# Performance work log

Measured on AMD Instinct MI355X. Metric: run time of the kernel, lower is better.

## Reference

```python
import math
import jax, jax.numpy as jnp
import numpy as np

B, S, DIM = 2, 4096, 512
HEADS, DIM_HEAD, CHUNK = 8, 64, 64
DIM_INNER = HEADS * DIM_HEAD
EPS = 1e-6


def rmsnorm(x, scale):
    var = jnp.mean(x * x, axis=-1, keepdims=True)
    return x * jax.lax.rsqrt(var + EPS) * scale


def mem_attn(p, x):
    # x: [c, dh] single chunk; tiny causal attention memory model
    q = x @ p['wq']
    k = x @ p['wk']
    v = x @ p['wv1']
    d = q.shape[-1]
    dots = (q @ k.T) * (d ** -0.5)
    c = x.shape[-2]
    mask = jnp.tril(jnp.ones((c, c), dtype=bool))
    dots = jnp.where(mask, dots, -1e9)
    attn = jax.nn.softmax(dots, axis=-1)
    hidden = attn @ v
    return jax.nn.silu(hidden) @ p['wv2']


def mem_loss(p, inp, tgt):
    pred = mem_attn(p, inp)
    return jnp.sum(jnp.mean((pred - tgt) ** 2, axis=-1))


def assoc_scan(gates, vals):
    # first-order linear recurrence y_t = g_t * y_{t-1} + v_t along axis=1
    def op(a, b):
        a1, b1 = a
        a2, b2 = b
        return a1 * a2, a2 * b1 + b2
    return jax.lax.associative_scan(op, (gates, vals), axis=1)


def setup_inputs():
    key = jax.random.key(0)
    ks = jax.random.split(key, 16)
    n = lambda k, shp, s: jax.random.normal(k, shp, dtype=jnp.float32) * s
    return {
        'seq': n(ks[0], (B, S, DIM), 1.0),
        'w_store_norm': jnp.ones((DIM,), jnp.float32),
        'w_retrieve_norm': jnp.ones((DIM,), jnp.float32),
        'w_post_norm': jnp.ones((DIM,), jnp.float32),
        'w_q': n(ks[1], (DIM, DIM_INNER), DIM ** -0.5),
        'w_kv': n(ks[2], (DIM, 2 * DIM_INNER), DIM ** -0.5),
        'w_step': n(ks[3], (DIM, HEADS), DIM ** -0.5),
        'w_mom': n(ks[4], (DIM, HEADS), DIM ** -0.5),
        'w_decay': n(ks[5], (DIM, HEADS), DIM ** -0.5),
        'w_combine': n(ks[6], (DIM_INNER, DIM), DIM_INNER ** -0.5),
        'wq': n(ks[7], (DIM_HEAD, DIM_HEAD), 0.01),
        'wk': n(ks[8], (DIM_HEAD, DIM_HEAD), 0.01),
        'wv1': n(ks[9], (DIM_HEAD, DIM_HEAD), 0.01),
        'wv2': n(ks[10], (DIM_HEAD, DIM_HEAD), 0.01),
    }


def reference(seq, w_store_norm, w_retrieve_norm, w_post_norm, w_q, w_kv,
              w_step, w_mom, w_decay, w_combine, wq, wk, wv1, wv2):
    b, s_len, d = seq.shape
    c, h, dh = CHUNK, HEADS, DIM_HEAD
    past = {'wq': wq, 'wk': wk, 'wv1': wv1, 'wv2': wv2}

    # ---------- store_memories ----------
    s = rmsnorm(seq, w_store_norm)
    n_full = (s_len // c) * c
    s = s[:, :n_full]
    nc = n_full // c

    # adaptive lr: [b,n,h] -> (b h) n -> chunk-mean [bh, nc]
    lr = jnp.exp(jax.nn.sigmoid(s @ w_step) * -15.0)
    lr = jnp.transpose(lr, (0, 2, 1)).reshape(b * h, nc, c).mean(-1)

    s_mean = s.reshape(b, nc, c, d).mean(2)  # [b, nc, d]
    mom_gate = jax.nn.sigmoid(s_mean @ w_mom)
    mom_gate = jnp.transpose(mom_gate, (0, 2, 1)).reshape(b * h, nc, 1)
    decay = jax.nn.sigmoid(s_mean @ w_decay)
    decay = jnp.transpose(decay, (0, 2, 1)).reshape(b * h, nc, 1)

    keys, values = jnp.split(s @ w_kv, 2, axis=-1)

    def chunkify(t):  # [b, n, h*dh] -> [(b h nc), c, dh]
        t = t.reshape(b, n_full, h, dh)
        t = jnp.transpose(t, (0, 2, 1, 3))
        return t.reshape(b * h * nc, c, dh)

    keys, values = chunkify(keys), chunkify(values)

    # per-chunk meta-gradients wrt shared memory-model params
    grads = jax.vmap(jax.grad(mem_loss), in_axes=(None, 0, 0))(past, keys, values)

    updates = {}
    for name in past:
        g = grads[name].reshape(b * h, nc, dh * dh)
        surprise = g * (-lr)[..., None]
        _, momentum = assoc_scan(mom_gate, surprise)
        _, upd = assoc_scan(1.0 - decay, momentum)
        updates[name] = upd.reshape(b * h, nc, dh, dh)

    wwu = {k2: past[k2][None, None] + updates[k2] for k2 in past}  # [bh, nc, dh, dh]

    # ---------- retrieve_memories ----------
    r = rmsnorm(seq, w_retrieve_norm)
    rc = r[:, c:]
    curtailed = s_len - c
    next_len = ((curtailed + 1 + c - 1) // c) * c
    pad = next_len - curtailed
    rc = jnp.pad(rc, ((0, 0), (0, pad), (0, 0)))

    q = rc @ w_q  # [b, next_len, h*dh]
    q = q.reshape(b, next_len, h, dh)
    q = jnp.transpose(q, (0, 2, 1, 3)).reshape(b * h * (next_len // c), c, dh)

    pc = {k2: v2.reshape(b * h * nc, dh, dh) for k2, v2 in wwu.items()}
    vals = jax.vmap(mem_attn)(pc, q)  # [(bh nc), c, dh]
    vals = vals.reshape(b, h, next_len, dh)
    vals = jnp.transpose(vals, (0, 2, 1, 3)).reshape(b, next_len, h * dh)
    vals = rmsnorm(vals @ w_combine, w_post_norm)
    vals = jnp.pad(vals, ((0, 0), (c, 0), (0, 0)))
    return vals[:, :-pad]
```

## Files before the change

kernel.cpp:

```cpp
#include <hip/hip_runtime.h>
#include <math.h>

constexpr int BATCH = 2, SEQ = 4096, DIM = 512, HEADS = 8, DH = 64, CH = 64;
constexpr int NC = SEQ / CH;
constexpr int BH = BATCH * HEADS;
constexpr int NCHUNK = BH * NC;
constexpr int ROWS = BATCH * SEQ;
constexpr int DI = HEADS * DH;
constexpr int TS = 64 * 72;

typedef __attribute__((ext_vector_type(8))) short short8;
typedef __attribute__((ext_vector_type(4))) short short4v;
typedef __attribute__((ext_vector_type(4))) float f32x4;

__device__ inline float sigmoidf_(float x){ return 1.f/(1.f+__expf(-x)); }
__device__ inline float dsilu_f(float x){ float s = sigmoidf_(x); return s*(1.f + x*(1.f-s)); }

__device__ inline unsigned short f2b(float f){
  union { float f; unsigned int u; } c; c.f = f;
  unsigned int u = c.u;
  unsigned int r = (u + 0x7FFFu + ((u >> 16) & 1u)) >> 16;
  return (unsigned short)r;
}
__device__ inline float b2f(unsigned short h){
// ... 12 lines not shown

template<bool SILUA>
__device__ inline void mm64(const unsigned short* A, const unsigned short* B,
                            f32x4 (&acc)[2], const MM& m)
{
  acc[0] = (f32x4){0.f,0.f,0.f,0.f};
  acc[1] = (f32x4){0.f,0.f,0.f,0.f};
  #pragma unroll
  for (int ks = 0; ks < 2; ks++){
    short8 a = *(const short8*)&A[(m.rowbase + m.lr)*72 + ks*32 + m.lg*8];
    if constexpr (SILUA){
      #pragma unroll
      for (int j = 0; j < 8; j++){
        float v = b2f((unsigned short)a[j]);
        v = v * sigmoidf_(v);
        a[j] = (short)f2b(v);
      }
    }
    #pragma unroll
    for (int ct = 0; ct < 2; ct++){
      short8 b = *(const short8*)&B[(m.colbase + ct*16 + m.lr)*72 + ks*32 + m.lg*8];
      acc[ct] = __builtin_amdgcn_mfma_f32_16x16x32_bf16(a, b, acc[ct], 0, 0, 0);
    }
  }
}

__device__ inline void storeN64(unsigned short* R, const f32x4 (&acc)[2], const MM& m, float scale){
  #pragma unroll
  for (int ct = 0; ct < 2; ct++){
    int c  = m.colbase + ct*16 + m.lr;
    int mb = m.rowbase + m.lg*4;
    #pragma unroll
    for (int r = 0; r < 4; r++) R[(mb+r)*72 + c] = f2b(acc[ct][r] * scale);
  }
}
__device__ inline void storeT64(unsigned short* T, const f32x4 (&acc)[2], const MM& m, float scale){
  #pragma unroll
  for (int ct = 0; ct < 2; ct++){
    int c  = m.colbase + ct*16 + m.lr;
    int mb = m.rowbase + m.lg*4;
    short4v p;
    #pragma unroll
    for (int r = 0; r < 4; r++) p[r] = (short)f2b(acc[ct][r] * scale);
    *(short4v*)&T[c*72 + mb] = p;
  }
}
__device__ inline void storeSC(float* S, const f32x4 (&acc)[2], const MM& m, float scale){
  #pragma unroll
  for (int ct = 0; ct < 2; ct++){
    int c  = m.colbase + ct*16 + m.lr;
    int mb = m.rowbase + m.lg*4;
    #pragma unroll
    for (int r = 0; r < 4; r++) S[(mb+r)*66 + c] = acc[ct][r] * scale;
  }
}
__device__ inline void storeGTb64(unsigned short* __restrict__ G, const f32x4 (&acc)[2],
                                  const MM& m, float scale){
  #pragma unroll
  for (int ct = 0; ct < 2; ct++){
    int c  = m.colbase + ct*16 + m.lr;
    int mb = m.rowbase + m.lg*4;
    short4v p;
    #pragma unroll
    for (int r = 0; r < 4; r++) p[r] = (short)f2b(acc[ct][r] * scale);
    *(short4v*)&G[c*64 + mb] = p;
  }
}

__device__ inline void loadTileBrow(unsigned short* R, const unsigned short* __restrict__ src,
                                    int stride, int tid){
  int i = tid >> 3, j8 = (tid & 7) * 8;
  *(short8*)&R[i*72 + j8] = *(const short8*)&src[(size_t)i*stride + j8];
}
__device__ inline void loadTileBrowT(unsigned short* R, unsigned short* T,
                                     const unsigned short* __restrict__ src,
                                     int stride, int tid){
  int i = tid >> 3, j8 = (tid & 7) * 8;
  short8 v = *(const short8*)&src[(size_t)i*stride + j8];
  *(short8*)&R[i*72 + j8] = v;
  #pragma unroll
  for (int jj = 0; jj < 8; jj++) T[(j8+jj)*72 + i] = (unsigned short)v[jj];
}

__global__ __launch_bounds__(256) void k_wprep_all(
    const float* __restrict__ w_kv, const float* __restrict__ w_q,
    const float* __restrict__ wcomb,
    const float* __restrict__ wq, const float* __restrict__ wk,
    const float* __restrict__ wv1, const float* __restrict__ wv2,
    unsigned short* __restrict__ wkvT_hi, unsigned short* __restrict__ wkvT_lo,
    unsigned short* __restrict__ wqT_hi, unsigned short* __restrict__ wcombT_hi,
    unsigned short* __restrict__ wpre)
{
  __shared__ float t[64][65];
  int blk = blockIdx.x;
  int tid = threadIdx.x;
  if (blk < 256){
    const float* src; unsigned short *dhi, *dlo;
    int R, C, bx, by;
    if (blk < 128){ src = w_kv;  dhi = wkvT_hi;  dlo = wkvT_lo; R = DIM; C = 2*DI; bx = blk & 15; by = blk >> 4; }
    else if (blk < 192){ int q = blk - 128; src = w_q;   dhi = wqT_hi;    dlo = nullptr; R = DIM; C = DI;  bx = q & 7; by = q >> 3; }
    else               { int q = blk - 192; src = wcomb; dhi = wcombT_hi; dlo = nullptr; R = DI;  C = DIM; bx = q & 7; by = q >> 3; }
    int c0 = bx * 64, r0 = by * 64;
    #pragma unroll
    for (int it = 0; it < 16; it++){
      int idx = it*256 + tid;
      int i = idx >> 6, j = idx & 63;
      t[i][j] = src[(size_t)(r0+i)*C + c0 + j];
    }
    __syncthreads();
    #pragma unroll
    for (int it = 0; it < 16; it++){
      int idx = it*256 + tid;
      int i = idx >> 6, j = idx & 63;
      float v = t[j][i];
      unsigned short hi = f2b(v);
      dhi[(size_t)(c0+i)*R + r0 + j] = hi;
      if (dlo) dlo[(size_t)(c0+i)*R + r0 + j] = f2b(v - b2f(hi));
    }
  } else {
    int b = blk - 256;
    const float* src = (b==0) ? wq : (b==1) ? wk : (b==2) ? wv1 : wv2;
    #pragma unroll
    for (int it = 0; it < 16; it++){
      int idx = it*256 + tid;
      int i = idx >> 6, j = idx & 63;
      t[i][j] = src[i*64 + j];
    }
    __syncthreads();
    #pragma unroll
    for (int it = 0; it < 16; it++){
      int idx = it*256 + tid;
      int i = idx >> 6, j = idx & 63;
      wpre[b*4096 + i*64 + j] = f2b(t[j][i]);
      if (b == 3) wpre[4*4096 + i*64 + j] = f2b(t[i][j]);
    }
  }
}

template<int MODE, bool LO>
__global__ __launch_bounds__(256, LO ? 2 : 4) void k_gemm3(
    const unsigned short* __restrict__ Ahg, const unsigned short* __restrict__ Alg,
    const unsigned short* __restrict__ Bhg, const unsigned short* __restrict__ Blg,
    float* __restrict__ Cf, unsigned short* __restrict__ Cb, int M, int N, int K)
{
  __shared__ __align__(16) unsigned short AhS[128*72];
  __shared__ __align__(16) unsigned short BhS[128*72];
  __shared__ __align__(16) unsigned short AlS[LO ? 128*72 : 8];
  __shared__ __align__(16) unsigned short BlS[LO ? 128*72 : 8];
  int tid = threadIdx.x;
  int nwg = gridDim.x * gridDim.y;
  int bid = blockIdx.y * gridDim.x + blockIdx.x;
  int swz = (bid & 7) * (nwg >> 3) + (bid >> 3);
  int m0 = (swz / gridDim.x) * 128;
  int n0 = (swz % gridDim.x) * 128;
  int wid = tid >> 6, lane = tid & 63;
  int lr = lane & 15, lg = lane >> 4;
  int wr = (wid >> 1) * 64, wc = (wid & 1) * 64;
  f32x4 acc[4][4];
  #pragma unroll
  for (int r = 0; r < 4; r++)
    #pragma unroll
    for (int c = 0; c < 4; c++) acc[r][c] = (f32x4){0.f,0.f,0.f,0.f};

  for (int k0 = 0; k0 < K; k0 += 64){
    #pragma unroll
    for (int it = 0; it < 4; it++){
      int idx = it*256 + tid;
      int row = idx >> 3, col8 = (idx & 7) * 8;
      size_t ga = (size_t)(m0+row)*K + k0 + col8;
      size_t gb = (size_t)(n0+row)*K + k0 + col8;
      *(short8*)&AhS[row*72 + col8] = *(const short8*)&Ahg[ga];
      *(short8*)&BhS[row*72 + col8] = *(const short8*)&Bhg[gb];
      if constexpr (LO){
        *(short8*)&AlS[row*72 + col8] = *(const short8*)&Alg[ga];
        *(short8*)&BlS[row*72 + col8] = *(const short8*)&Blg[gb];
      }
    }
    __syncthreads();
    #pragma unroll
    for (int ks = 0; ks < 2; ks++){
      short8 ah[4], al[4], bh[4], bl[4];
      #pragma unroll
      for (int i = 0; i < 4; i++){
        int ao = (wr + i*16 + lr)*72 + ks*32 + lg*8;
        int bo = (wc + i*16 + lr)*72 + ks*32 + lg*8;
        ah[i] = *(const short8*)&AhS[ao];
        bh[i] = *(const short8*)&BhS[bo];
        if constexpr (LO){
          al[i] = *(const short8*)&AlS[ao];
          bl[i] = *(const short8*)&BlS[bo];
        }
      }
      #pragma unroll
      for (int r = 0; r < 4; r++)
        #pragma unroll
        for (int c = 0; c < 4; c++){
          acc[r][c] = __builtin_amdgcn_mfma_f32_16x16x32_bf16(ah[r], bh[c], acc[r][c], 0, 0, 0);
          if constexpr (LO){
            acc[r][c] = __builtin_amdgcn_mfma_f32_16x16x32_bf16(ah[r], bl[c], acc[r][c], 0, 0, 0);
            acc[r][c] = __builtin_amdgcn_mfma_f32_16x16x32_bf16(al[r], bh[c], acc[r][c], 0, 0, 0);
          }
        }
    }
    __syncthreads();
  }
  #pragma unroll
  for (int rt = 0; rt < 4; rt++)
    #pragma unroll
    for (int ct = 0; ct < 4; ct++){
      int col = n0 + wc + ct*16 + lr;
      int rowb = m0 + wr + rt*16 + lg*4;
      #pragma unroll
      for (int r = 0; r < 4; r++){
        float v = acc[rt][ct][r];
        if constexpr (MODE == 0) Cf[(size_t)(rowb+r)*N + col] = v;
        if constexpr (MODE == 1) Cb[(size_t)(rowb+r)*N + col] = f2b(v);
      }
    }
}

__global__ __launch_bounds__(256, 4) void k_gemm1_dual(
    const unsigned short* __restrict__ A0, const unsigned short* __restrict__ B0,
    unsigned short* __restrict__ C0,
    const unsigned short* __restrict__ A1, const unsigned short* __restrict__ B1,
    unsigned short* __restrict__ C1, int M, int N, int K)
{
  __shared__ __align__(16) unsigned short AhS[128*72];
  __shared__ __align__(16) unsigned short BhS[128*72];
  const unsigned short* Ahg = blockIdx.z ? A1 : A0;
  const unsigned short* Bhg = blockIdx.z ? B1 : B0;
  unsigned short* Cb        = blockIdx.z ? C1 : C0;
  int tid = threadIdx.x;
  int nwg = gridDim.x * gridDim.y;
  int bid = blockIdx.y * gridDim.x + blockIdx.x;
  int swz = (bid & 7) * (nwg >> 3) + (bid >> 3);
  int m0 = (swz / gridDim.x) * 128;
  int n0 = (swz % gridDim.x) * 128;
  int wid = tid >> 6, lane = tid & 63;
  int lr = lane & 15, lg = lane >> 4;
  int wr = (wid >> 1) * 64, wc = (wid & 1) * 64;
  f32x4 acc[4][4];
  #pragma unroll
  for (int r = 0; r < 4; r++)
    #pragma unroll
    for (int c = 0; c < 4; c++) acc[r][c] = (f32x4){0.f,0.f,0.f,0.f};

  for (int k0 = 0; k0 < K; k0 += 64){
    #pragma unroll
    for (int it = 0; it < 4; it++){
      int idx = it*256 + tid;
      int row = idx >> 3, col8 = (idx & 7) * 8;
      *(short8*)&AhS[row*72 + col8] = *(const short8*)&Ahg[(size_t)(m0+row)*K + k0 + col8];
      *(short8*)&BhS[row*72 + col8] = *(const short8*)&Bhg[(size_t)(n0+row)*K + k0 + col8];
    }
    __syncthreads();
    #pragma unroll
    for (int ks = 0; ks < 2; ks++){
      short8 ah[4], bh[4];
      #pragma unroll
      for (int i = 0; i < 4; i++){
        ah[i] = *(const short8*)&AhS[(wr + i*16 + lr)*72 + ks*32 + lg*8];
        bh[i] = *(const short8*)&BhS[(wc + i*16 + lr)*72 + ks*32 + lg*8];
      }
      #pragma unroll
      for (int r = 0; r < 4; r++)
        #pragma unroll
        for (int c = 0; c < 4; c++)
          acc[r][c] = __builtin_amdgcn_mfma_f32_16x16x32_bf16(ah[r], bh[c], acc[r][c], 0, 0, 0);
    }
    __syncthreads();
  }
  #pragma unroll
  for (int rt = 0; rt < 4; rt++)
    #pragma unroll
    for (int ct = 0; ct < 4; ct++){
      int col = n0 + wc + ct*16 + lr;
      int rowb = m0 + wr + rt*16 + lg*4;
      #pragma unroll
      for (int r = 0; r < 4; r++)
        Cb[(size_t)(rowb+r)*N + col] = f2b(acc[rt][ct][r]);
    }
}

__global__ __launch_bounds__(256) void k_store_norm(
    const float* __restrict__ seq, const float* __restrict__ wsn,
    const float* __restrict__ wrn, const float* __restrict__ wstep,
    unsigned short* __restrict__ s_hi, unsigned short* __restrict__ s_lo,
    unsigned short* __restrict__ rq_hi, float* __restrict__ lrp)
{
  int wid = threadIdx.x >> 6, lane = threadIdx.x & 63;
  int row = blockIdx.x * 4 + wid;
  int b = row >> 12, t = row & 4095;
  const float* x = seq + (size_t)row * DIM;
  float4 v0 = *(const float4*)&x[lane*4];
  float4 v1 = *(const float4*)&x[256 + lane*4];
  float xv[8] = {v0.x, v0.y, v0.z, v0.w, v1.x, v1.y, v1.z, v1.w};
  float ss = 0.f;
  #pragma unroll
  for (int j = 0; j < 8; j++) ss += xv[j]*xv[j];
  #pragma unroll
  for (int m = 1; m < 64; m <<= 1) ss += __shfl_xor(ss, m);
  float rinv = rsqrtf(ss * (1.f/DIM) + 1e-6f);

  float4 w0 = *(const float4*)&wsn[lane*4];
  float4 w1 = *(const float4*)&wsn[256 + lane*4];
  float wv[8] = {w0.x, w0.y, w0.z, w0.w, w1.x, w1.y, w1.z, w1.w};
  float sv[8];
  short4v h0, h1, l0, l1;
  #pragma unroll
  for (int j = 0; j < 8; j++){
    sv[j] = xv[j] * rinv * wv[j];
    unsigned short hi = f2b(sv[j]);
    unsigned short lo = f2b(sv[j] - b2f(hi));
    if (j < 4){ h0[j] = (short)hi; l0[j] = (short)lo; }
    else      { h1[j-4] = (short)hi; l1[j-4] = (short)lo; }
  }
  size_t sbase = (size_t)row*DIM + lane*4;
  *(short4v*)&s_hi[sbase] = h0; *(short4v*)&s_hi[sbase + 256] = h1;
  *(short4v*)&s_lo[sbase] = l0; *(short4v*)&s_lo[sbase + 256] = l1;

  if (t >= CH){
    float4 r0 = *(const float4*)&wrn[lane*4];
    float4 r1 = *(const float4*)&wrn[256 + lane*4];
    float rv[8] = {r0.x, r0.y, r0.z, r0.w, r1.x, r1.y, r1.z, r1.w};
    short4v rh0, rh1;
    #pragma unroll
    for (int j = 0; j < 8; j++){
      float q = xv[j] * rinv * rv[j];
      unsigned short hi = f2b(q);
      if (j < 4) rh0[j] = (short)hi; else rh1[j-4] = (short)hi;
    }
    size_t rbase = ((size_t)b*SEQ + (t - CH))*DIM + lane*4;
    *(short4v*)&rq_hi[rbase] = rh0; *(short4v*)&rq_hi[rbase + 256] = rh1;
  } else {
    short4v z; z[0]=0; z[1]=0; z[2]=0; z[3]=0;
    size_t rbase = ((size_t)b*SEQ + (SEQ - CH + t))*DIM + lane*4;
    *(short4v*)&rq_hi[rbase] = z; *(short4v*)&rq_hi[rbase + 256] = z;
  }

  float acc[8] = {0.f,0.f,0.f,0.f,0.f,0.f,0.f,0.f};
  #pragma unroll
  for (int j = 0; j < 8; j++){
    int e = (j < 4) ? (lane*4 + j) : (256 + lane*4 + (j-4));
    float4 wa = *(const float4*)&wstep[e*8];
    float4 wb = *(const float4*)&wstep[e*8 + 4];
    acc[0] += sv[j]*wa.x; acc[1] += sv[j]*wa.y; acc[2] += sv[j]*wa.z; acc[3] += sv[j]*wa.w;
    acc[4] += sv[j]*wb.x; acc[5] += sv[j]*wb.y; acc[6] += sv[j]*wb.z; acc[7] += sv[j]*wb.w;
  }
  #pragma unroll
  for (int m = 1; m < 64; m <<= 1){
    #pragma unroll
    for (int h = 0; h < 8; h++) acc[h] += __shfl_xor(acc[h], m);
  }
  float a = acc[0];
  #pragma unroll
  for (int h = 1; h < 8; h++) a = (lane == h) ? acc[h] : a;
  if (lane < 8)
    lrp[(size_t)row*HEADS + lane] = __expf(-15.f * sigmoidf_(a));
}

__global__ __launch_bounds__(256) void k_stats(
    const unsigned short* __restrict__ s_hi,
    const float* __restrict__ lrp,
    const float* __restrict__ wmom, const float* __restrict__ wdec,
    float* __restrict__ mg, float* __restrict__ dec, float* __restrict__ lrc)
{
  __shared__ float smean[DIM];
  int blk = blockIdx.x;
  int b = blk >> 6, ch = blk & 63;
  int tid = threadIdx.x;
  size_t off = ((size_t)(b*SEQ + ch*CH)) * DIM;
  for (int e = tid; e < DIM; e += 256){
    float acc = 0.f;
    for (int i = 0; i < CH; i++)
      acc += b2f(s_hi[off + (size_t)i*DIM + e]);
    smean[e] = acc * (1.f/CH);
  }
  __syncthreads();
  int gh = tid >> 5, l = tid & 31;
  float am = 0.f, ad = 0.f;
  for (int e = l; e < DIM; e += 32){
    float v = smean[e];
    am += v * wmom[e*HEADS + gh];
    ad += v * wdec[e*HEADS + gh];
  }
  const float* lrbase = lrp + ((size_t)(b*SEQ + ch*CH)) * HEADS + gh;
  float al = lrbase[(size_t)l*HEADS] + lrbase[(size_t)(l+32)*HEADS];
  #pragma unroll
  for (int m = 1; m < 32; m <<= 1){
    am += __shfl_xor(am, m);
    ad += __shfl_xor(ad, m);
    al += __shfl_xor(al, m);
  }
  if (l == 0){
    int o = (b*HEADS + gh)*NC + ch;
    mg[o]  = sigmoidf_(am);
    dec[o] = sigmoidf_(ad);
    lrc[o] = al * (1.f/CH);
  }
}

__global__ __launch_bounds__(512) void k_grads(
    const unsigned short* __restrict__ kvb, const float* __restrict__ kvv,
    const unsigned short* __restrict__ wpre,
    const float* __restrict__ lrc, unsigned short* __restrict__ g)
{
  __shared__ __align__(16) unsigned short sm[12*TS];
  __shared__ __align__(16) float SC[64*66];
  unsigned short *Xr = sm,        *XT = sm + TS,
                 *s2 = sm + 2*TS, *s3 = sm + 3*TS, *s4 = sm + 4*TS,
                 *s5 = sm + 5*TS, *s6 = sm + 6*TS, *s7 = sm + 7*TS,
                 *s8 = sm + 8*TS, *s9 = sm + 9*TS, *s10 = sm + 10*TS,
                 *s11 = sm + 11*TS;
  unsigned short *SCu = (unsigned short*)SC;
  int chunk = blockIdx.x;
  int bh = chunk >> 6, t = chunk & 63;
  int b = bh >> 3, h = bh & 7;
  int tid = threadIdx.x;
  MM M = mmctx();
  const unsigned short* xb = kvb + ((size_t)(b*SEQ + t*CH)) * DI + h*DH;
  const float* tbase = kvv + ((size_t)(b*SEQ + t*CH)) * DI + h*DH;
  float negLr = -lrc[bh*NC + t];
  f32x4 acc[2], accV[2];

  loadTileBrowT(Xr, XT, xb, DI, tid);
  loadTileBrow(s2, wpre + 0*4096, 64, tid);
  loadTileBrow(s3, wpre + 1*4096, 64, tid);
  loadTileBrow(s4, wpre + 2*4096, 64, tid);
  loadTileBrow(s5, wpre + 3*4096, 64, tid);
  loadTileBrow(s6, wpre + 4*4096, 64, tid);
  __syncthreads();
  mm64<false>(Xr, s2, acc, M);
  storeN64(s7, acc, M, 1.f); storeT64(s8, acc, M, 1.f);
  mm64<false>(Xr, s3, acc, M);
  storeN64(s9, acc, M, 1.f); storeT64(s10, acc, M, 1.f);
  mm64<false>(Xr, s4, accV, M);
  storeN64(s11, accV, M, 1.f);
  __syncthreads();
  storeT64(s2, accV, M, 1.f);
  mm64<false>(s7, s9, acc, M);
  storeSC(SC, acc, M, 0.125f);
  __syncthreads();
  {
    int row = tid >> 3, q = tid & 7;
    float p[8];
    float mx = -1e30f;
    #pragma unroll
    for (int cc = 0; cc < 8; cc++){
      int col = q*8 + cc;
      float x = SC[row*66 + col];
      p[cc] = (col <= row) ? x : -1e9f;
      mx = fmaxf(mx, p[cc]);
    }
    mx = fmaxf(mx, __shfl_xor(mx, 1));
    mx = fmaxf(mx, __shfl_xor(mx, 2));
    mx = fmaxf(mx, __shfl_xor(mx, 4));
    float sum = 0.f;
    #pragma unroll
    for (int cc = 0; cc < 8; cc++){ p[cc] = __expf(p[cc] - mx); sum += p[cc]; }
    sum += __shfl_xor(sum, 1);
    sum += __shfl_xor(sum, 2);
    sum += __shfl_xor(sum, 4);
    float inv = 1.f / sum;
    #pragma unroll
    for (int cc = 0; cc < 8; cc++){
      int col = q*8 + cc;
      unsigned short hh = f2b(p[cc] * inv);
      s7[row*72 + col] = hh;
      s9[col*72 + row] = hh;
    }
  }
  __syncthreads();
  mm64<false>(s7, s2, acc, M);
  storeN64(s3, acc, M, 1.f); storeT64(s4, acc, M, 1.f);
  __syncthreads();
  mm64<true>(s3, s5, acc, M);
  #pragma unroll
  for (int ct = 0; ct < 2; ct++){
    int c  = M.colbase + ct*16 + M.lr;
    int mb = M.rowbase + M.lg*4;
    #pragma unroll
    for (int r = 0; r < 4; r++){
// ... 159 lines not shown
    #pragma unroll
    for (int r = 0; r < 4; r++){
      size_t o = ((size_t)(b*SEQ + t*CH + mb + r))*DI + h*DH + c;
      vals_hi[o] = f2b(acc[ct][r]);
    }
  }
}

__global__ __launch_bounds__(256) void k_outnorm(
    const unsigned short* __restrict__ tmp, const float* __restrict__ wpn,
    float* __restrict__ out)
{
  int wid = threadIdx.x >> 6, lane = threadIdx.x & 63;
  int row = blockIdx.x * 4 + wid;
  int b = row >> 12, r = row & 4095;
  float* dst = out + ((size_t)b*SEQ + r) * DIM;
  if (r < CH){
    float4 z = make_float4(0.f, 0.f, 0.f, 0.f);
    *(float4*)&dst[lane*8] = z;
    *(float4*)&dst[lane*8 + 4] = z;
    return;
  }
  const unsigned short* src = tmp + ((size_t)b*SEQ + (r - CH)) * DIM;
  short8 t0 = *(const short8*)&src[lane*8];
  float xv[8];
  #pragma unroll
  for (int j = 0; j < 8; j++) xv[j] = b2f((unsigned short)t0[j]);
  float ss = 0.f;
  #pragma unroll
  for (int j = 0; j < 8; j++) ss += xv[j]*xv[j];
  #pragma unroll
  for (int m = 1; m < 64; m <<= 1) ss += __shfl_xor(ss, m);
  float rinv = rsqrtf(ss * (1.f/DIM) + 1e-6f);
  float4 o0, o1;
  o0.x = xv[0]*rinv*wpn[lane*8+0]; o0.y = xv[1]*rinv*wpn[lane*8+1];
  o0.z = xv[2]*rinv*wpn[lane*8+2]; o0.w = xv[3]*rinv*wpn[lane*8+3];
  o1.x = xv[4]*rinv*wpn[lane*8+4]; o1.y = xv[5]*rinv*wpn[lane*8+5];
  o1.z = xv[6]*rinv*wpn[lane*8+6]; o1.w = xv[7]*rinv*wpn[lane*8+7];
  *(float4*)&dst[lane*8] = o0;
  *(float4*)&dst[lane*8 + 4] = o1;
}

extern "C" void kernel_launch(void* const* d_in, const int* in_sizes, int n_in,
                              void* d_out, int out_size, void* d_ws, size_t ws_size,
                              hipStream_t stream)
{
  (void)in_sizes; (void)n_in; (void)ws_size; (void)out_size;
  const float* seq   = (const float*)d_in[0];
  const float* wsn   = (const float*)d_in[1];
  const float* wrn   = (const float*)d_in[2];
  const float* wpn   = (const float*)d_in[3];
  const float* w_q   = (const float*)d_in[4];
  const float* w_kv  = (const float*)d_in[5];
  const float* wstep = (const float*)d_in[6];
  const float* wmom  = (const float*)d_in[7];
  const float* wdec  = (const float*)d_in[8];
  const float* wcomb = (const float*)d_in[9];
  const float* wq    = (const float*)d_in[10];
  const float* wk    = (const float*)d_in[11];
  const float* wv1   = (const float*)d_in[12];
  const float* wv2   = (const float*)d_in[13];
  float* out = (float*)d_out;

  char* p = (char*)d_ws;
  unsigned short* s_hi  = (unsigned short*)p; p += (size_t)ROWS*DIM*2;
  unsigned short* s_lo  = (unsigned short*)p; p += (size_t)ROWS*DIM*2;
  unsigned short* rq_hi = (unsigned short*)p; p += (size_t)ROWS*DIM*2;
  unsigned short* kvb   = (unsigned short*)p; p += (size_t)ROWS*DI*2;
  float* kvv            = (float*)p;          p += (size_t)ROWS*DI*4;
  unsigned short* qb    = (unsigned short*)p; p += (size_t)ROWS*DI*2;
  unsigned short* g     = (unsigned short*)p; p += (size_t)4*NCHUNK*4096*2;
  float* lrp            = (float*)p;          p += (size_t)ROWS*HEADS*4;
  float* mg             = (float*)p;          p += (size_t)BH*NC*4;
  float* dec            = (float*)p;          p += (size_t)BH*NC*4;
  float* lrc            = (float*)p;          p += (size_t)BH*NC*4;
  unsigned short* wkvT_hi   = (unsigned short*)p; p += (size_t)(2*DI)*DIM*2;
  unsigned short* wkvT_lo   = (unsigned short*)p; p += (size_t)(2*DI)*DIM*2;
  unsigned short* wqT_hi    = (unsigned short*)p; p += (size_t)DI*DIM*2;
  unsigned short* wcombT_hi = (unsigned short*)p; p += (size_t)DIM*DI*2;
  unsigned short* wpre      = (unsigned short*)p; p += (size_t)5*4096*2;
  unsigned short* vals_hi   = (unsigned short*)p; p += (size_t)ROWS*DI*2;
  unsigned short* tmp = s_hi;

  k_wprep_all<<<260, 256, 0, stream>>>(w_kv, w_q, wcomb, wq, wk, wv1, wv2,
                                       wkvT_hi, wkvT_lo, wqT_hi, wcombT_hi, wpre);

  k_store_norm<<<ROWS/4, 256, 0, stream>>>(seq, wsn, wrn, wstep, s_hi, s_lo, rq_hi, lrp);
  k_gemm1_dual<<<dim3(DI/128, ROWS/128, 2), 256, 0, stream>>>(
      s_hi, wkvT_hi, kvb, rq_hi, wqT_hi, qb, ROWS, DI, DIM);
  k_gemm3<0,true><<<dim3(DI/128, ROWS/128), 256, 0, stream>>>(
      s_hi, s_lo, wkvT_hi + (size_t)DI*DIM, wkvT_lo + (size_t)DI*DIM,
      kvv, nullptr, ROWS, DI, DIM);
  k_stats<<<BATCH*NC, 256, 0, stream>>>(s_hi, lrp, wmom, wdec, mg, dec, lrc);
  k_grads<<<NCHUNK, 512, 0, stream>>>(kvb, kvv, wpre, lrc, g);
  k_scan<<<(4*BH*2048)/256, 256, 0, stream>>>(g, mg, dec, wq, wk, wv1, wv2);
  k_retrieve<<<NCHUNK, 512, 0, stream>>>(qb, g, vals_hi);
  k_gemm3<1,false><<<dim3(DIM/128, ROWS/128), 256, 0, stream>>>(
      vals_hi, nullptr, wcombT_hi, nullptr, nullptr, tmp, ROWS, DIM, DI);
  k_outnorm<<<ROWS/4, 256, 0, stream>>>(tmp, wpn, out);
}
```

Baseline: 175.6 us.

## Merge front-end prep kernels and mid-stage GEMMs plus stats into fewer launches

Merges weight prep and the store/retrieve RMSnorm kernel into one launch, and folds the two bf16 projection GEMMs, the split-precision kv GEMM and the chunk-stats kernel into a single k_mid launch selected by blockIdx.z. This removes three kernel launches and their gaps, and lets independent work share the device. In exchange, all k_mid variants now allocate the larger LDS footprint and use launch bounds of 2 blocks, which can lower occupancy for the plain GEMMs, and the LO choice becomes a runtime branch instead of a template parameter.

```diff
diff --git a/kernel.cpp b/kernel.cpp
--- a/kernel.cpp
+++ b/kernel.cpp
@@ -118,71 +118,276 @@
   for (int jj = 0; jj < 8; jj++) T[(j8+jj)*72 + i] = (unsigned short)v[jj];
 }
 
-__global__ __launch_bounds__(256) void k_wprep_all(
+__global__ __launch_bounds__(256) void k_front(
+    const float* __restrict__ seq, const float* __restrict__ wsn,
+    const float* __restrict__ wrn, const float* __restrict__ wstep,
     const float* __restrict__ w_kv, const float* __restrict__ w_q,
     const float* __restrict__ wcomb,
     const float* __restrict__ wq, const float* __restrict__ wk,
     const float* __restrict__ wv1, const float* __restrict__ wv2,
+    unsigned short* __restrict__ s_hi, unsigned short* __restrict__ s_lo,
+    unsigned short* __restrict__ rq_hi, float* __restrict__ lrp,
     unsigned short* __restrict__ wkvT_hi, unsigned short* __restrict__ wkvT_lo,
     unsigned short* __restrict__ wqT_hi, unsigned short* __restrict__ wcombT_hi,
     unsigned short* __restrict__ wpre)
 {
   __shared__ float t[64][65];
-  int blk = blockIdx.x;
   int tid = threadIdx.x;
-  if (blk < 256){
-    const float* src; unsigned short *dhi, *dlo;
-    int R, C, bx, by;
-    if (blk < 128){ src = w_kv;  dhi = wkvT_hi;  dlo = wkvT_lo; R = DIM; C = 2*DI; bx = blk & 15; by = blk >> 4; }
-    else if (blk < 192){ int q = blk - 128; src = w_q;   dhi = wqT_hi;    dlo = nullptr; R = DIM; C = DI;  bx = q & 7; by = q >> 3; }
-    else               { int q = blk - 192; src = wcomb; dhi = wcombT_hi; dlo = nullptr; R = DI;  C = DIM; bx = q & 7; by = q >> 3; }
-    int c0 = bx * 64, r0 = by * 64;
-    #pragma unroll
-    for (int it = 0; it < 16; it++){
-      int idx = it*256 + tid;
-      int i = idx >> 6, j = idx & 63;
-      t[i][j] = src[(size_t)(r0+i)*C + c0 + j];
-    }
-    __syncthreads();
-    #pragma unroll
-    for (int it = 0; it < 16; it++){
-      int idx = it*256 + tid;
-      int i = idx >> 6, j = idx & 63;
-      float v = t[j][i];
-      unsigned short hi = f2b(v);
-      dhi[(size_t)(c0+i)*R + r0 + j] = hi;
-      if (dlo) dlo[(size_t)(c0+i)*R + r0 + j] = f2b(v - b2f(hi));
-    }
+  if (blockIdx.x >= ROWS/4){
+    int blk = blockIdx.x - ROWS/4;
+    if (blk < 256){
+      const float* src; unsigned short *dhi, *dlo;
+      int R, C, bx, by;
+      if (blk < 128){ src = w_kv;  dhi = wkvT_hi;  dlo = wkvT_lo; R = DIM; C = 2*DI; bx = blk & 15; by = blk >> 4; }
+      else if (blk < 192){ int q = blk - 128; src = w_q;   dhi = wqT_hi;    dlo = nullptr; R = DIM; C = DI;  bx = q & 7; by = q >> 3; }
+      else               { int q = blk - 192; src = wcomb; dhi = wcombT_hi; dlo = nullptr; R = DI;  C = DIM; bx = q & 7; by = q >> 3; }
+      int c0 = bx * 64, r0 = by * 64;
+      #pragma unroll
+      for (int it = 0; it < 16; it++){
+        int idx = it*256 + tid;
+        int i = idx >> 6, j = idx & 63;
+        t[i][j] = src[(size_t)(r0+i)*C + c0 + j];
+      }
+      __syncthreads();
+      #pragma unroll
+      for (int it = 0; it < 16; it++){
+        int idx = it*256 + tid;
+        int i = idx >> 6, j = idx & 63;
+        float v = t[j][i];
+        unsigned short hi = f2b(v);
+        dhi[(size_t)(c0+i)*R + r0 + j] = hi;
+        if (dlo) dlo[(size_t)(c0+i)*R + r0 + j] = f2b(v - b2f(hi));
+      }
+    } else {
+      int b = blk - 256;
+      const float* src = (b==0) ? wq : (b==1) ? wk : (b==2) ? wv1 : wv2;
+      #pragma unroll
+      for (int it = 0; it < 16; it++){
+        int idx = it*256 + tid;
+        int i = idx >> 6, j = idx & 63;
+        t[i][j] = src[i*64 + j];
+      }
+      __syncthreads();
+      #pragma unroll
+      for (int it = 0; it < 16; it++){
+        int idx = it*256 + tid;
+        int i = idx >> 6, j = idx & 63;
+        wpre[b*4096 + i*64 + j] = f2b(t[j][i]);
+        if (b == 3) wpre[4*4096 + i*64 + j] = f2b(t[i][j]);
+      }
+    }
+    return;
+  }
+  int wid = tid >> 6, lane = tid & 63;
+  int row = blockIdx.x * 4 + wid;
+  int b = row >> 12, tt = row & 4095;
+  const float* x = seq + (size_t)row * DIM;
+  float4 v0 = *(const float4*)&x[lane*4];
+  float4 v1 = *(const float4*)&x[256 + lane*4];
+  float xv[8] = {v0.x, v0.y, v0.z, v0.w, v1.x, v1.y, v1.z, v1.w};
+  float ss = 0.f;
+  #pragma unroll
+  for (int j = 0; j < 8; j++) ss += xv[j]*xv[j];
+  #pragma unroll
+  for (int m = 1; m < 64; m <<= 1) ss += __shfl_xor(ss, m);
+  float rinv = rsqrtf(ss * (1.f/DIM) + 1e-6f);
+
+  float4 w0 = *(const float4*)&wsn[lane*4];
+  float4 w1 = *(const float4*)&wsn[256 + lane*4];
+  float wv[8] = {w0.x, w0.y, w0.z, w0.w, w1.x, w1.y, w1.z, w1.w};
+  float sv[8];
+  short4v h0, h1, l0, l1;
+  #pragma unroll
+  for (int j = 0; j < 8; j++){
+    sv[j] = xv[j] * rinv * wv[j];
+    unsigned short hi = f2b(sv[j]);
+    unsigned short lo = f2b(sv[j] - b2f(hi));
+    if (j < 4){ h0[j] = (short)hi; l0[j] = (short)lo; }
+    else      { h1[j-4] = (short)hi; l1[j-4] = (short)lo; }
+  }
+  size_t sbase = (size_t)row*DIM + lane*4;
+  *(short4v*)&s_hi[sbase] = h0; *(short4v*)&s_hi[sbase + 256] = h1;
+  *(short4v*)&s_lo[sbase] = l0; *(short4v*)&s_lo[sbase + 256] = l1;
+
+  if (tt >= CH){
+    float4 r0 = *(const float4*)&wrn[lane*4];
+    float4 r1 = *(const float4*)&wrn[256 + lane*4];
+    float rv[8] = {r0.x, r0.y, r0.z, r0.w, r1.x, r1.y, r1.z, r1.w};
+    short4v rh0, rh1;
+    #pragma unroll
+    for (int j = 0; j < 8; j++){
+      float q = xv[j] * rinv * rv[j];
+      unsigned short hi = f2b(q);
+      if (j < 4) rh0[j] = (short)hi; else rh1[j-4] = (short)hi;
+    }
+    size_t rbase = ((size_t)b*SEQ + (tt - CH))*DIM + lane*4;
+    *(short4v*)&rq_hi[rbase] = rh0; *(short4v*)&rq_hi[rbase + 256] = rh1;
   } else {
-    int b = blk - 256;
-    const float* src = (b==0) ? wq : (b==1) ? wk : (b==2) ? wv1 : wv2;
-    #pragma unroll
-    for (int it = 0; it < 16; it++){
-      int idx = it*256 + tid;
-      int i = idx >> 6, j = idx & 63;
-      t[i][j] = src[i*64 + j];
-    }
-    __syncthreads();
-    #pragma unroll
-    for (int it = 0; it < 16; it++){
-      int idx = it*256 + tid;
-      int i = idx >> 6, j = idx & 63;
-      wpre[b*4096 + i*64 + j] = f2b(t[j][i]);
-      if (b == 3) wpre[4*4096 + i*64 + j] = f2b(t[i][j]);
-    }
-  }
-}
-
-template<int MODE, bool LO>
-__global__ __launch_bounds__(256, LO ? 2 : 4) void k_gemm3(
-    const unsigned short* __restrict__ Ahg, const unsigned short* __restrict__ Alg,
-    const unsigned short* __restrict__ Bhg, const unsigned short* __restrict__ Blg,
-    float* __restrict__ Cf, unsigned short* __restrict__ Cb, int M, int N, int K)
+    short4v z; z[0]=0; z[1]=0; z[2]=0; z[3]=0;
+    size_t rbase = ((size_t)b*SEQ + (SEQ - CH + tt))*DIM + lane*4;
+    *(short4v*)&rq_hi[rbase] = z; *(short4v*)&rq_hi[rbase + 256] = z;
+  }
+
+  float acc[8] = {0.f,0.f,0.f,0.f,0.f,0.f,0.f,0.f};
+  #pragma unroll
+  for (int j = 0; j < 8; j++){
+    int e = (j < 4) ? (lane*4 + j) : (256 + lane*4 + (j-4));
+    float4 wa = *(const float4*)&wstep[e*8];
+    float4 wb = *(const float4*)&wstep[e*8 + 4];
+    acc[0] += sv[j]*wa.x; acc[1] += sv[j]*wa.y; acc[2] += sv[j]*wa.z; acc[3] += sv[j]*wa.w;
+    acc[4] += sv[j]*wb.x; acc[5] += sv[j]*wb.y; acc[6] += sv[j]*wb.z; acc[7] += sv[j]*wb.w;
+  }
+  #pragma unroll
+  for (int m = 1; m < 64; m <<= 1){
+    #pragma unroll
+    for (int h = 0; h < 8; h++) acc[h] += __shfl_xor(acc[h], m);
+  }
+  float a = acc[0];
+  #pragma unroll
+  for (int h = 1; h < 8; h++) a = (lane == h) ? acc[h] : a;
+  if (lane < 8)
+    lrp[(size_t)row*HEADS + lane] = __expf(-15.f * sigmoidf_(a));
+}
+
+__global__ __launch_bounds__(256, 2) void k_mid(
+    const unsigned short* __restrict__ s_hi, const unsigned short* __restrict__ s_lo,
+    const unsigned short* __restrict__ rq_hi,
+    const unsigned short* __restrict__ wkvT_hi, const unsigned short* __restrict__ wkvT_lo,
+    const unsigned short* __restrict__ wqT_hi,
+    unsigned short* __restrict__ kvb, unsigned short* __restrict__ qb,
+    float* __restrict__ kvv,
+    const float* __restrict__ lrp, const float* __restrict__ wmom,
+    const float* __restrict__ wdec,
+    float* __restrict__ mg, float* __restrict__ dec, float* __restrict__ lrc)
 {
   __shared__ __align__(16) unsigned short AhS[128*72];
   __shared__ __align__(16) unsigned short BhS[128*72];
-  __shared__ __align__(16) unsigned short AlS[LO ? 128*72 : 8];
-  __shared__ __align__(16) unsigned short BlS[LO ? 128*72 : 8];
+  __shared__ __align__(16) unsigned short AlS[128*72];
+  __shared__ __align__(16) unsigned short BlS[128*72];
+  int tid = threadIdx.x;
+  int z = blockIdx.z;
+  if (z == 3){
+    int bid = blockIdx.y * gridDim.x + blockIdx.x;
+    if (bid >= BATCH*NC) return;
+    float* smean = (float*)AhS;
+    int b = bid >> 6, ch = bid & 63;
+    size_t off = ((size_t)(b*SEQ + ch*CH)) * DIM;
+    for (int e = tid; e < DIM; e += 256){
+      float acc = 0.f;
+      for (int i = 0; i < CH; i++)
+        acc += b2f(s_hi[off + (size_t)i*DIM + e]);
+      smean[e] = acc * (1.f/CH);
+    }
+    __syncthreads();
+    int gh = tid >> 5, l = tid & 31;
+    float am = 0.f, ad = 0.f;
+    for (int e = l; e < DIM; e += 32){
+      float v = smean[e];
+      am += v * wmom[e*HEADS + gh];
+      ad += v * wdec[e*HEADS + gh];
+    }
+    const float* lrbase = lrp + ((size_t)(b*SEQ + ch*CH)) * HEADS + gh;
+    float al = lrbase[(size_t)l*HEADS] + lrbase[(size_t)(l+32)*HEADS];
+    #pragma unroll
+    for (int m = 1; m < 32; m <<= 1){
+      am += __shfl_xor(am, m);
+      ad += __shfl_xor(ad, m);
+      al += __shfl_xor(al, m);
+    }
+    if (l == 0){
+      int o = (b*HEADS + gh)*NC + ch;
+      mg[o]  = sigmoidf_(am);
+      dec[o] = sigmoidf_(ad);
+      lrc[o] = al * (1.f/CH);
+    }
+    return;
+  }
+  const bool LO = (z == 2);
+  const unsigned short* Ahg = (z == 1) ? rq_hi : s_hi;
+  const unsigned short* Alg = s_lo;
+  const unsigned short* Bhg = (z == 0) ? wkvT_hi : (z == 1) ? wqT_hi
+                                       : wkvT_hi + (size_t)DI*DIM;
+  const unsigned short* Blg = wkvT_lo + (size_t)DI*DIM;
+  const int M = ROWS, N = DI, K = DIM;
+
+  int nwg = gridDim.x * gridDim.y;
+  int bid = blockIdx.y * gridDim.x + blockIdx.x;
+  int swz = (bid & 7) * (nwg >> 3) + (bid >> 3);
+  int m0 = (swz / gridDim.x) * 128;
+  int n0 = (swz % gridDim.x) * 128;
+  int wid = tid >> 6, lane = tid & 63;
+  int lr = lane & 15, lg = lane >> 4;
+  int wr = (wid >> 1) * 64, wc = (wid & 1) * 64;
+  f32x4 acc[4][4];
+  #pragma unroll
+  for (int r = 0; r < 4; r++)
+    #pragma unroll
+    for (int c = 0; c < 4; c++) acc[r][c] = (f32x4){0.f,0.f,0.f,0.f};
+
+  for (int k0 = 0; k0 < K; k0 += 64){
+    #pragma unroll
+    for (int it = 0; it < 4; it++){
+      int idx = it*256 + tid;
+      int row = idx >> 3, col8 = (idx & 7) * 8;
+      size_t ga = (size_t)(m0+row)*K + k0 + col8;
+      size_t gb = (size_t)(n0+row)*K + k0 + col8;
+      *(short8*)&AhS[row*72 + col8] = *(const short8*)&Ahg[ga];
+      *(short8*)&BhS[row*72 + col8] = *(const short8*)&Bhg[gb];
+      if (LO){
+        *(short8*)&AlS[row*72 + col8] = *(const short8*)&Alg[ga];
+        *(short8*)&BlS[row*72 + col8] = *(const short8*)&Blg[gb];
+      }
+    }
+    __syncthreads();
+    #pragma unroll
+    for (int ks = 0; ks < 2; ks++){
+      short8 ah[4], al[4], bh[4], bl[4];
+      #pragma unroll
+      for (int i = 0; i < 4; i++){
+        int ao = (wr + i*16 + lr)*72 + ks*32 + lg*8;
+        int bo = (wc + i*16 + lr)*72 + ks*32 + lg*8;
+        ah[i] = *(const short8*)&AhS[ao];
+        bh[i] = *(const short8*)&BhS[bo];
+        if (LO){
+          al[i] = *(const short8*)&AlS[ao];
+          bl[i] = *(const short8*)&BlS[bo];
+        }
+      }
+      #pragma unroll
+      for (int r = 0; r < 4; r++)
+        #pragma unroll
+        for (int c = 0; c < 4; c++){
+          acc[r][c] = __builtin_amdgcn_mfma_f32_16x16x32_bf16(ah[r], bh[c], acc[r][c], 0, 0, 0);
+          if (LO){
+            acc[r][c] = __builtin_amdgcn_mfma_f32_16x16x32_bf16(ah[r], bl[c], acc[r][c], 0, 0, 0);
+            acc[r][c] = __builtin_amdgcn_mfma_f32_16x16x32_bf16(al[r], bh[c], acc[r][c], 0, 0, 0);
+          }
+        }
+    }
+    __syncthreads();
+  }
+  unsigned short* Cb = (z == 1) ? qb : kvb;
+  #pragma unroll
+  for (int rt = 0; rt < 4; rt++)
+    #pragma unroll
+    for (int ct = 0; ct < 4; ct++){
+      int col = n0 + wc + ct*16 + lr;
+      int rowb = m0 + wr + rt*16 + lg*4;
+      #pragma unroll
+      for (int r = 0; r < 4; r++){
+        float v = acc[rt][ct][r];
+        if (LO) kvv[(size_t)(rowb+r)*N + col] = v;
+        else    Cb[(size_t)(rowb+r)*N + col] = f2b(v);
+      }
+    }
+}
+
+__global__ __launch_bounds__(256, 4) void k_gemm1(
+    const unsigned short* __restrict__ Ahg, const unsigned short* __restrict__ Bhg,
+    unsigned short* __restrict__ Cb, int M, int N, int K)
+{
+  __shared__ __align__(16) unsigned short AhS[128*72];
+  __shared__ __align__(16) unsigned short BhS[128*72];
   int tid = threadIdx.x;
   int nwg = gridDim.x * gridDim.y;
   int bid = blockIdx.y * gridDim.x + blockIdx.x;
@@ -203,89 +408,6 @@
     for (int it = 0; it < 4; it++){
       int idx = it*256 + tid;
       int row = idx >> 3, col8 = (idx & 7) * 8;
-      size_t ga = (size_t)(m0+row)*K + k0 + col8;
-      size_t gb = (size_t)(n0+row)*K + k0 + col8;
-      *(short8*)&AhS[row*72 + col8] = *(const short8*)&Ahg[ga];
-      *(short8*)&BhS[row*72 + col8] = *(const short8*)&Bhg[gb];
-      if constexpr (LO){
-        *(short8*)&AlS[row*72 + col8] = *(const short8*)&Alg[ga];
-        *(short8*)&BlS[row*72 + col8] = *(const short8*)&Blg[gb];
-      }
-    }
-    __syncthreads();
-    #pragma unroll
-    for (int ks = 0; ks < 2; ks++){
-      short8 ah[4], al[4], bh[4], bl[4];
-      #pragma unroll
-      for (int i = 0; i < 4; i++){
-        int ao = (wr + i*16 + lr)*72 + ks*32 + lg*8;
-        int bo = (wc + i*16 + lr)*72 + ks*32 + lg*8;
-        ah[i] = *(const short8*)&AhS[ao];
-        bh[i] = *(const short8*)&BhS[bo];
-        if constexpr (LO){
-          al[i] = *(const short8*)&AlS[ao];
-          bl[i] = *(const short8*)&BlS[bo];
-        }
-      }
-      #pragma unroll
-      for (int r = 0; r < 4; r++)
-        #pragma unroll
-        for (int c = 0; c < 4; c++){
-          acc[r][c] = __builtin_amdgcn_mfma_f32_16x16x32_bf16(ah[r], bh[c], acc[r][c], 0, 0, 0);
-          if constexpr (LO){
-            acc[r][c] = __builtin_amdgcn_mfma_f32_16x16x32_bf16(ah[r], bl[c], acc[r][c], 0, 0, 0);
-            acc[r][c] = __builtin_amdgcn_mfma_f32_16x16x32_bf16(al[r], bh[c], acc[r][c], 0, 0, 0);
-          }
-        }
-    }
-    __syncthreads();
-  }
-  #pragma unroll
-  for (int rt = 0; rt < 4; rt++)
-    #pragma unroll
-    for (int ct = 0; ct < 4; ct++){
-      int col = n0 + wc + ct*16 + lr;
-      int rowb = m0 + wr + rt*16 + lg*4;
-      #pragma unroll
-      for (int r = 0; r < 4; r++){
-        float v = acc[rt][ct][r];
-        if constexpr (MODE == 0) Cf[(size_t)(rowb+r)*N + col] = v;
-        if constexpr (MODE == 1) Cb[(size_t)(rowb+r)*N + col] = f2b(v);
-      }
-    }
-}
-
-__global__ __launch_bounds__(256, 4) void k_gemm1_dual(
-    const unsigned short* __restrict__ A0, const unsigned short* __restrict__ B0,
-    unsigned short* __restrict__ C0,
-    const unsigned short* __restrict__ A1, const unsigned short* __restrict__ B1,
-    unsigned short* __restrict__ C1, int M, int N, int K)
-{
-  __shared__ __align__(16) unsigned short AhS[128*72];
-  __shared__ __align__(16) unsigned short BhS[128*72];
-  const unsigned short* Ahg = blockIdx.z ? A1 : A0;
-  const unsigned short* Bhg = blockIdx.z ? B1 : B0;
-  unsigned short* Cb        = blockIdx.z ? C1 : C0;
-  int tid = threadIdx.x;
-  int nwg = gridDim.x * gridDim.y;
-  int bid = blockIdx.y * gridDim.x + blockIdx.x;
-  int swz = (bid & 7) * (nwg >> 3) + (bid >> 3);
-  int m0 = (swz / gridDim.x) * 128;
-  int n0 = (swz % gridDim.x) * 128;
-  int wid = tid >> 6, lane = tid & 63;
-  int lr = lane & 15, lg = lane >> 4;
-  int wr = (wid >> 1) * 64, wc = (wid & 1) * 64;
-  f32x4 acc[4][4];
-  #pragma unroll
-  for (int r = 0; r < 4; r++)
-    #pragma unroll
-    for (int c = 0; c < 4; c++) acc[r][c] = (f32x4){0.f,0.f,0.f,0.f};
-
-  for (int k0 = 0; k0 < K; k0 += 64){
-    #pragma unroll
-    for (int it = 0; it < 4; it++){
-      int idx = it*256 + tid;
-      int row = idx >> 3, col8 = (idx & 7) * 8;
       *(short8*)&AhS[row*72 + col8] = *(const short8*)&Ahg[(size_t)(m0+row)*K + k0 + col8];
       *(short8*)&BhS[row*72 + col8] = *(const short8*)&Bhg[(size_t)(n0+row)*K + k0 + col8];
     }
@@ -316,124 +438,6 @@
       for (int r = 0; r < 4; r++)
         Cb[(size_t)(rowb+r)*N + col] = f2b(acc[rt][ct][r]);
     }
-}
-
-__global__ __launch_bounds__(256) void k_store_norm(
-    const float* __restrict__ seq, const float* __restrict__ wsn,
-    const float* __restrict__ wrn, const float* __restrict__ wstep,
-    unsigned short* __restrict__ s_hi, unsigned short* __restrict__ s_lo,
-    unsigned short* __restrict__ rq_hi, float* __restrict__ lrp)
-{
-  int wid = threadIdx.x >> 6, lane = threadIdx.x & 63;
-  int row = blockIdx.x * 4 + wid;
-  int b = row >> 12, t = row & 4095;
-  const float* x = seq + (size_t)row * DIM;
-  float4 v0 = *(const float4*)&x[lane*4];
-  float4 v1 = *(const float4*)&x[256 + lane*4];
-  float xv[8] = {v0.x, v0.y, v0.z, v0.w, v1.x, v1.y, v1.z, v1.w};
-  float ss = 0.f;
-  #pragma unroll
-  for (int j = 0; j < 8; j++) ss += xv[j]*xv[j];
-  #pragma unroll
-  for (int m = 1; m < 64; m <<= 1) ss += __shfl_xor(ss, m);
-  float rinv = rsqrtf(ss * (1.f/DIM) + 1e-6f);
-
-  float4 w0 = *(const float4*)&wsn[lane*4];
-  float4 w1 = *(const float4*)&wsn[256 + lane*4];
-  float wv[8] = {w0.x, w0.y, w0.z, w0.w, w1.x, w1.y, w1.z, w1.w};
-  float sv[8];
-  short4v h0, h1, l0, l1;
-  #pragma unroll
-  for (int j = 0; j < 8; j++){
-    sv[j] = xv[j] * rinv * wv[j];
-    unsigned short hi = f2b(sv[j]);
-    unsigned short lo = f2b(sv[j] - b2f(hi));
-    if (j < 4){ h0[j] = (short)hi; l0[j] = (short)lo; }
-    else      { h1[j-4] = (short)hi; l1[j-4] = (short)lo; }
-  }
-  size_t sbase = (size_t)row*DIM + lane*4;
-  *(short4v*)&s_hi[sbase] = h0; *(short4v*)&s_hi[sbase + 256] = h1;
-  *(short4v*)&s_lo[sbase] = l0; *(short4v*)&s_lo[sbase + 256] = l1;
-
-  if (t >= CH){
-    float4 r0 = *(const float4*)&wrn[lane*4];
-    float4 r1 = *(const float4*)&wrn[256 + lane*4];
-    float rv[8] = {r0.x, r0.y, r0.z, r0.w, r1.x, r1.y, r1.z, r1.w};
-    short4v rh0, rh1;
-    #pragma unroll
-    for (int j = 0; j < 8; j++){
-      float q = xv[j] * rinv * rv[j];
-      unsigned short hi = f2b(q);
-      if (j < 4) rh0[j] = (short)hi; else rh1[j-4] = (short)hi;
-    }
-    size_t rbase = ((size_t)b*SEQ + (t - CH))*DIM + lane*4;
-    *(short4v*)&rq_hi[rbase] = rh0; *(short4v*)&rq_hi[rbase + 256] = rh1;
-  } else {
-    short4v z; z[0]=0; z[1]=0; z[2]=0; z[3]=0;
-    size_t rbase = ((size_t)b*SEQ + (SEQ - CH + t))*DIM + lane*4;
-    *(short4v*)&rq_hi[rbase] = z; *(short4v*)&rq_hi[rbase + 256] = z;
-  }
-
-  float acc[8] = {0.f,0.f,0.f,0.f,0.f,0.f,0.f,0.f};
-  #pragma unroll
-  for (int j = 0; j < 8; j++){
-    int e = (j < 4) ? (lane*4 + j) : (256 + lane*4 + (j-4));
-    float4 wa = *(const float4*)&wstep[e*8];
-    float4 wb = *(const float4*)&wstep[e*8 + 4];
-    acc[0] += sv[j]*wa.x; acc[1] += sv[j]*wa.y; acc[2] += sv[j]*wa.z; acc[3] += sv[j]*wa.w;
-    acc[4] += sv[j]*wb.x; acc[5] += sv[j]*wb.y; acc[6] += sv[j]*wb.z; acc[7] += sv[j]*wb.w;
-  }
-  #pragma unroll
-  for (int m = 1; m < 64; m <<= 1){
-    #pragma unroll
-    for (int h = 0; h < 8; h++) acc[h] += __shfl_xor(acc[h], m);
-  }
-  float a = acc[0];
-  #pragma unroll
-  for (int h = 1; h < 8; h++) a = (lane == h) ? acc[h] : a;
-  if (lane < 8)
-    lrp[(size_t)row*HEADS + lane] = __expf(-15.f * sigmoidf_(a));
-}
-
-__global__ __launch_bounds__(256) void k_stats(
-    const unsigned short* __restrict__ s_hi,
-    const float* __restrict__ lrp,
-    const float* __restrict__ wmom, const float* __restrict__ wdec,
-    float* __restrict__ mg, float* __restrict__ dec, float* __restrict__ lrc)
-{
-  __shared__ float smean[DIM];
-  int blk = blockIdx.x;
-  int b = blk >> 6, ch = blk & 63;
-  int tid = threadIdx.x;
-  size_t off = ((size_t)(b*SEQ + ch*CH)) * DIM;
-  for (int e = tid; e < DIM; e += 256){
-    float acc = 0.f;
-    for (int i = 0; i < CH; i++)
-      acc += b2f(s_hi[off + (size_t)i*DIM + e]);
-    smean[e] = acc * (1.f/CH);
-  }
-  __syncthreads();
-  int gh = tid >> 5, l = tid & 31;
-  float am = 0.f, ad = 0.f;
-  for (int e = l; e < DIM; e += 32){
-    float v = smean[e];
-    am += v * wmom[e*HEADS + gh];
-    ad += v * wdec[e*HEADS + gh];
-  }
-  const float* lrbase = lrp + ((size_t)(b*SEQ + ch*CH)) * HEADS + gh;
-  float al = lrbase[(size_t)l*HEADS] + lrbase[(size_t)(l+32)*HEADS];
-  #pragma unroll
-  for (int m = 1; m < 32; m <<= 1){
-    am += __shfl_xor(am, m);
-    ad += __shfl_xor(ad, m);
-    al += __shfl_xor(al, m);
-  }
-  if (l == 0){
-    int o = (b*HEADS + gh)*NC + ch;
-    mg[o]  = sigmoidf_(am);
-    dec[o] = sigmoidf_(ad);
-    lrc[o] = al * (1.f/CH);
-  }
 }
 
 __global__ __launch_bounds__(512) void k_grads(
@@ -759,20 +763,16 @@
   unsigned short* vals_hi   = (unsigned short*)p; p += (size_t)ROWS*DI*2;
   unsigned short* tmp = s_hi;
 
-  k_wprep_all<<<260, 256, 0, stream>>>(w_kv, w_q, wcomb, wq, wk, wv1, wv2,
-                                       wkvT_hi, wkvT_lo, wqT_hi, wcombT_hi, wpre);
-
-  k_store_norm<<<ROWS/4, 256, 0, stream>>>(seq, wsn, wrn, wstep, s_hi, s_lo, rq_hi, lrp);
-  k_gemm1_dual<<<dim3(DI/128, ROWS/128, 2), 256, 0, stream>>>(
-      s_hi, wkvT_hi, kvb, rq_hi, wqT_hi, qb, ROWS, DI, DIM);
-  k_gemm3<0,true><<<dim3(DI/128, ROWS/128), 256, 0, stream>>>(
-      s_hi, s_lo, wkvT_hi + (size_t)DI*DIM, wkvT_lo + (size_t)DI*DIM,
-      kvv, nullptr, ROWS, DI, DIM);
-  k_stats<<<BATCH*NC, 256, 0, stream>>>(s_hi, lrp, wmom, wdec, mg, dec, lrc);
+  k_front<<<ROWS/4 + 260, 256, 0, stream>>>(
+      seq, wsn, wrn, wstep, w_kv, w_q, wcomb, wq, wk, wv1, wv2,
+      s_hi, s_lo, rq_hi, lrp, wkvT_hi, wkvT_lo, wqT_hi, wcombT_hi, wpre);
+  k_mid<<<dim3(DI/128, ROWS/128, 4), 256, 0, stream>>>(
+      s_hi, s_lo, rq_hi, wkvT_hi, wkvT_lo, wqT_hi,
+      kvb, qb, kvv, lrp, wmom, wdec, mg, dec, lrc);
   k_grads<<<NCHUNK, 512, 0, stream>>>(kvb, kvv, wpre, lrc, g);
   k_scan<<<(4*BH*2048)/256, 256, 0, stream>>>(g, mg, dec, wq, wk, wv1, wv2);
   k_retrieve<<<NCHUNK, 512, 0, stream>>>(qb, g, vals_hi);
-  k_gemm3<1,false><<<dim3(DIM/128, ROWS/128), 256, 0, stream>>>(
-      vals_hi, nullptr, wcombT_hi, nullptr, nullptr, tmp, ROWS, DIM, DI);
+  k_gemm1<<<dim3(DIM/128, ROWS/128), 256, 0, stream>>>(
+      vals_hi, wcombT_hi, tmp, ROWS, DIM, DI);
   k_outnorm<<<ROWS/4, 256, 0, stream>>>(tmp, wpn, out);
 }
```

Result: no change. 174.4 us (-0.7%).
